# Optimization experiments

Hardware: AMD Instinct MI355X
Metric: run time of the kernel (lower is better)

Reference implementation:

```python
import jax, jax.numpy as jnp
import numpy as np

CUR, FULL, BS, DIM, H, D = 512, 1024, 4, 1024, 16, 64
PREV = FULL - CUR


def _rel_shift(x):
    # x: (cur, full, bs, h) -- TransformerXL relative shift (pad/reshape/slice)
    cur, full = x.shape[0], x.shape[1]
    zero_pad = jnp.zeros((cur, 1) + x.shape[2:], x.dtype)
    x_padded = jnp.concatenate([zero_pad, x], axis=1)           # (cur, full+1, bs, h)
    x_padded = x_padded.reshape((full + 1, cur) + x.shape[2:])  # view trick
    x = x_padded[1:].reshape(x.shape)
    tri = jnp.tril(jnp.ones((cur, full), x.dtype), full - cur)  # keep valid band
    return x * tri[:, :, None, None]


def setup_inputs() -> dict:
    key = jax.random.key(0)
    ks = jax.random.split(key, 12)
    s = jnp.float32(0.02)
    # causal mask: query i (at absolute pos i+PREV) may not attend to key j > i+PREV
    mask = (jnp.arange(FULL)[None, :] > (jnp.arange(CUR)[:, None] + PREV))[:, :, None]
    return {
        "inputs": jax.random.normal(ks[0], (CUR, BS, DIM), jnp.float32),
        "pos_embedding": jax.random.normal(ks[1], (FULL, 1, DIM), jnp.float32),
        "full_input": jax.random.normal(ks[2], (FULL, BS, DIM), jnp.float32),
        "u": jax.random.normal(ks[3], (H, D), jnp.float32) * s,
        "v": jax.random.normal(ks[4], (H, D), jnp.float32) * s,
        "W_kv": jax.random.normal(ks[5], (DIM, 2 * H * D), jnp.float32) * s,
        "b_kv": jnp.zeros((2 * H * D,), jnp.float32),
        "W_q": jax.random.normal(ks[6], (DIM, H * D), jnp.float32) * s,
        "b_q": jnp.zeros((H * D,), jnp.float32),
        "W_pos": jax.random.normal(ks[7], (DIM, H * D), jnp.float32) * s,
        "b_pos": jnp.zeros((H * D,), jnp.float32),
        "W_proj": jax.random.normal(ks[8], (H * D, DIM), jnp.float32) * s,
        "b_proj": jnp.zeros((DIM,), jnp.float32),
        "mask": mask,
    }


def reference(inputs, pos_embedding, full_input, u, v, W_kv, b_kv, W_q, b_q,
              W_pos, b_pos, W_proj, b_proj, mask):
    cur_seq, bs = inputs.shape[0], inputs.shape[1]
    full_seq = full_input.shape[0]
    scale = jnp.float32(1.0 / D ** 0.5)

    kv = full_input @ W_kv + b_kv                       # (full, bs, 2*H*D)
    key, value = jnp.split(kv, 2, axis=-1)
    query = inputs @ W_q + b_q                          # (cur, bs, H*D)
    r = (pos_embedding @ W_pos + b_pos).reshape(full_seq, H, D)

    key = key.reshape(full_seq, bs, H, D)
    value = value.reshape(full_seq, bs, H, D)
    query = query.reshape(cur_seq, bs, H, D)

    content_attn = jnp.einsum('ibhd,jbhd->ijbh', query + u, key)
    position_attn = jnp.einsum('ibhd,jhd->ijbh', query + v, r)
    position_attn = _rel_shift(position_attn)

    attn = (content_attn + position_attn) * scale       # (cur, full, bs, h)
    attn = jnp.where(mask[:, :, :, None], -jnp.inf, attn)
    attn = jax.nn.softmax(attn, axis=1)                 # softmax over full_seq

    attn_vec = jnp.einsum('ijbh,jbhd->ibhd', attn, value)
    attn_vec = attn_vec.reshape(cur_seq, bs, H * D)
    return attn_vec @ W_proj + b_proj                   # (cur, bs, DIM)
```

## Files before the change

kernel.cpp:

```cpp
#include <hip/hip_runtime.h>


typedef unsigned short u16;
typedef short short8 __attribute__((ext_vector_type(8)));
typedef float f32x4 __attribute__((ext_vector_type(4)));

#define BSZ 4
#define PREV 512

__device__ __forceinline__ float b2f(u16 u) {
  union { unsigned int i; float f; } x; x.i = ((unsigned int)u) << 16; return x.f;
}
__device__ __forceinline__ u16 f2b(float f) {
  union { float f; unsigned int i; } x; x.f = f;
  unsigned int u = x.i;
  return (u16)((u + 0x7fffu + ((u >> 16) & 1u)) >> 16);
}
__device__ __forceinline__ void storeC(u16* C, size_t idx, float v) { C[idx] = f2b(v); }
__device__ __forceinline__ void storeC(float* C, size_t idx, float v) { C[idx] = v; }

__device__ __forceinline__ void load_lds16(const u16* g, void* l) {
  __builtin_amdgcn_global_load_lds(
      (const __attribute__((address_space(1))) unsigned int*)g,
      (__attribute__((address_space(3))) unsigned int*)l, 16, 0, 0);
}

__global__ __launch_bounds__(256)
void prep(const float* __restrict__ s0, const float* __restrict__ s1,
          const float* __restrict__ s2, u16* __restrict__ d0,
          u16* __restrict__ d1, u16* __restrict__ d2,
          const float* __restrict__ W0, const float* __restrict__ W1,
          const float* __restrict__ W2, const float* __restrict__ W3,
          u16* __restrict__ T0, u16* __restrict__ T1,
          u16* __restrict__ T2, u16* __restrict__ T3) {
  __shared__ u16 ld[64 * 66];
  const int bxg = blockIdx.x;
  if (bxg < 3584) {
    const float* s; u16* d; size_t base;
    if (bxg < 2048)      { s = s0; d = d0; base = (size_t)bxg * 2048; }
    else if (bxg < 3072) { s = s1; d = d1; base = (size_t)(bxg - 2048) * 2048; }
    else                 { s = s2; d = d2; base = (size_t)(bxg - 3072) * 2048; }
    size_t i = base + (size_t)threadIdx.x * 8;
    const f32x4* p = reinterpret_cast<const f32x4*>(s + i);
    f32x4 a = p[0], b = p[1];
    short8 r;
#pragma unroll
    for (int e = 0; e < 4; e++) { r[e] = (short)f2b(a[e]); r[e + 4] = (short)f2b(b[e]); }
    *reinterpret_cast<short8*>(d + i) = r;
    return;
  }
  const int l = bxg - 3584;
  const int z = l >> 9;
  const int rem = l & 511;
  const int bx = rem & 31, by = rem >> 5;
  const float* W; u16* T; int N;
  if (z == 0)      { W = W0; T = T0; N = 2048; }
  else if (z == 1) { W = W1; T = T1; N = 1024; }
  else if (z == 2) { W = W2; T = T2; N = 1024; }
  else             { W = W3; T = T3; N = 1024; }
  const int K = 1024;
  const int n0 = bx * 64, k0 = by * 64;
  if (n0 >= N) return;

  const int tid = threadIdx.x;
#pragma unroll
  for (int rep = 0; rep < 16; rep++) {
    int idx = tid + 256 * rep;
    int kk = idx >> 6, nn = idx & 63;
    ld[kk * 66 + nn] = f2b(W[(size_t)(k0 + kk) * N + n0 + nn]);
  }
  __syncthreads();
#pragma unroll
  for (int rep = 0; rep < 16; rep++) {
    int idx = tid + 256 * rep;
    int nn = idx >> 6, kk = idx & 63;
    T[(size_t)(n0 + nn) * K + k0 + kk] = ld[kk * 66 + nn];
  }
}

template <typename OT, int MODE>
__device__ __forceinline__ void gemm_core(
    short* __restrict__ at, short* __restrict__ bt,
    const u16* __restrict__ A, const u16* __restrict__ BT,
    const float* __restrict__ bias, OT* __restrict__ C, u16* __restrict__ C2,
    int N, int K, int bx, int by)
{
  const int tid = threadIdx.x;
  const int lane = tid & 63, w = tid >> 6;
  const int wr = w >> 1, wc = w & 1;
  const int quad = lane >> 4, ml = lane & 15;
  const int row0 = by * 128, col0 = bx * 128;

  const int srow = lane & 15;
  const int skoff = (lane >> 4) * 8;

  f32x4 acc[4][4];
  const f32x4 fzero = {0.f, 0.f, 0.f, 0.f};
#pragma unroll
  for (int i = 0; i < 4; i++)
#pragma unroll
    for (int j = 0; j < 4; j++) acc[i][j] = fzero;

  for (int k0 = 0; k0 < K; k0 += 64) {
    __syncthreads();
#pragma unroll
    for (int i = 0; i < 4; i++) {
      int c = 4 * w + i;
      int mc = c >> 1, kc = c & 1;
      load_lds16(A + (size_t)(row0 + mc * 16 + srow) * K + k0 + kc * 32 + skoff,
                 (void*)(at + c * 512));
      load_lds16(BT + (size_t)(col0 + mc * 16 + srow) * K + k0 + kc * 32 + skoff,
                 (void*)(bt + c * 512));
    }
    __syncthreads();

    short8 af[4][2], bf[4][2];
#pragma unroll
    for (int mc = 0; mc < 4; mc++)
#pragma unroll
      for (int kc = 0; kc < 2; kc++)
        af[mc][kc] = *reinterpret_cast<const short8*>(at + ((((wr * 4 + mc) * 2 + kc) * 64) + lane) * 8);
#pragma unroll
    for (int nc = 0; nc < 4; nc++)
#pragma unroll
      for (int kc = 0; kc < 2; kc++)
        bf[nc][kc] = *reinterpret_cast<const short8*>(bt + ((((wc * 4 + nc) * 2 + kc) * 64) + lane) * 8);

#pragma unroll
    for (int mc = 0; mc < 4; mc++)
#pragma unroll
      for (int nc = 0; nc < 4; nc++)
#pragma unroll
        for (int kc = 0; kc < 2; kc++)
          acc[mc][nc] = __builtin_amdgcn_mfma_f32_16x16x32_bf16(af[mc][kc], bf[nc][kc], acc[mc][nc], 0, 0, 0);
  }

#pragma unroll
  for (int nc = 0; nc < 4; nc++) {
    int col = col0 + wc * 64 + nc * 16 + ml;
    float bv = bias[col];
#pragma unroll
    for (int mc = 0; mc < 4; mc++) {
#pragma unroll
      for (int reg = 0; reg < 4; reg++) {
        int row = row0 + wr * 64 + mc * 16 + quad * 4 + reg;
        float val = acc[mc][nc][reg] + bv;
        if constexpr (MODE == 0) {
          storeC(C, (size_t)row * N + col, val);
        } else if constexpr (MODE == 1) {
          int j = row >> 2, bb = row & 3;
          int tile = j >> 6, jl = j & 63;
          if (col < 1024) {
            int h = col >> 6, d = col & 63;
            int ncj = jl >> 4, nlj = jl & 15, kcd = d >> 5, qdd = (d >> 3) & 3, jjd = d & 7;
            C[((size_t)(bb * 16 + h) * 16 + tile) * 4096 +
              ((ncj * 2 + kcd) * 64 + qdd * 16 + nlj) * 8 + jjd] = f2b(val);
          } else {
            int c2 = col - 1024;
            int h = c2 >> 6, d = c2 & 63;
            int ncd = d >> 4, nld = d & 15, kcj = jl >> 5, qdj = (jl >> 3) & 3, jjj = jl & 7;
            C2[((size_t)(bb * 16 + h) * 16 + tile) * 4096 +
               ((kcj * 4 + ncd) * 64 + qdj * 16 + nld) * 8 + jjj] = f2b(val);
          }
        } else {
          int h = col >> 6, d = col & 63;
          C[((size_t)h * 1024 + row) * 64 + d] = f2b(val);
        }
      }
    }
  }
}

__global__ __launch_bounds__(256, 2)
void gemm3(const u16* __restrict__ fibf, const u16* __restrict__ WkvT,
           const float* __restrict__ b_kv, u16* __restrict__ Kt2, u16* __restrict__ Vt2,
           const u16* __restrict__ inbf, const u16* __restrict__ WqT,
           const float* __restrict__ b_q, u16* __restrict__ qq,
           const u16* __restrict__ pebf, const u16* __restrict__ WposT,
           const float* __restrict__ b_pos, u16* __restrict__ Rt)
{
  __shared__ __align__(16) short at[8192];
  __shared__ __align__(16) short bt[8192];
  const int id = blockIdx.x;
  if (id < 512) {
    gemm_core<u16, 1>(at, bt, fibf, WkvT, b_kv, Kt2, Vt2, 2048, 1024, id & 15, id >> 4);
  } else if (id < 640) {
    const int l = id - 512;
    gemm_core<u16, 0>(at, bt, inbf, WqT, b_q, qq, (u16*)nullptr, 1024, 1024, l & 7, l >> 3);
  } else {
    const int l = id - 640;
    gemm_core<u16, 2>(at, bt, pebf, WposT, b_pos, Rt, (u16*)nullptr, 1024, 1024, l & 7, l >> 3);
  }
}

__global__ __launch_bounds__(256, 2)
void gemm_proj(const u16* __restrict__ A, const u16* __restrict__ BT,
               const float* __restrict__ bias, float* __restrict__ C)
{
  __shared__ __align__(16) short at[8192];
  __shared__ __align__(16) short bt[8192];
  gemm_core<float, 0>(at, bt, A, BT, bias, C, (u16*)nullptr, 1024, 1024,
                      blockIdx.x, blockIdx.y);
}

__global__ __launch_bounds__(256, 4)
void flash_xl(const u16* __restrict__ q, const u16* __restrict__ Kt2,
              const u16* __restrict__ Vt2, const u16* __restrict__ Rt,
              const float* __restrict__ u, const float* __restrict__ v,
              float* __restrict__ po, float* __restrict__ pm,
              float* __restrict__ pl)
{
  __shared__ __align__(16) short kb[4096];
  __shared__ __align__(16) short vb[4096];
  __shared__ __align__(16) short pt[4][1024];

  const int tid = threadIdx.x, lane = tid & 63, w = tid >> 6;
  const int quad = lane >> 4, ml = lane & 15;
  const int x = blockIdx.x;
  int it, s, nseg;
  if (x < 12) { int g = x / 3; it = 7 - g; s = x - g * 3; nseg = 3; }
  else        { int y = x - 12; it = 3 - (y >> 1); s = y & 1; nseg = 2; }
  const int nt = it + 9;
  const int qn = (nseg == 3) ? (nt / 3) : (nt >> 1);
  const int rn = nt - qn * nseg;
  const int ts = s * qn + (s < rn ? s : rn);
  const int te = ts + qn + (s < rn ? 1 : 0);

  const int b = blockIdx.y, h = blockIdx.z;
  const int bh = b * 16 + h;
  const int i0 = it * 64, ig0 = i0 + w * 16;

  const u16* Kbase = Kt2 + ((size_t)(b * 16 + h) * 16) * 4096;
  const u16* Vbase = Vt2 + ((size_t)(b * 16 + h) * 16) * 4096;
  const u16* Rp = Rt + (size_t)h * 65536;

  short8 qu[2], qvf[2];
  {
    int ig = ig0 + ml;
#pragma unroll
    for (int kc = 0; kc < 2; kc++) {
      int dbase = kc * 32 + quad * 8;
      short8 qq = *reinterpret_cast<const short8*>(q + ((size_t)ig * BSZ + b) * 1024 + h * 64 + dbase);
      const f32x4* up = reinterpret_cast<const f32x4*>(u + h * 64 + dbase);
      const f32x4* vp = reinterpret_cast<const f32x4*>(v + h * 64 + dbase);
      f32x4 u0 = up[0], u1 = up[1], v0 = vp[0], v1 = vp[1];
#pragma unroll
      for (int e = 0; e < 8; e++) {
        float qf = b2f((u16)qq[e]);
        float uu = (e < 4) ? u0[e] : u1[e - 4];
        float vv = (e < 4) ? v0[e] : v1[e - 4];
        qu[kc][e]  = (short)f2b((qf + uu) * 0.125f);
        qvf[kc][e] = (short)f2b((qf + vv) * 0.125f);
      }
    }
  }

  const f32x4 fzero = {0.f, 0.f, 0.f, 0.f};
  f32x4 o_acc[4];
#pragma unroll
  for (int i = 0; i < 4; i++) o_acc[i] = fzero;
  float m_run[4], l_run[4];
#pragma unroll
  for (int i = 0; i < 4; i++) { m_run[i] = -1e30f; l_run[i] = 0.f; }

  short8 pk0, pk1, pv0, pv1;
  {
    const u16* kg = Kbase + (size_t)ts * 4096;
    const u16* vg = Vbase + (size_t)ts * 4096;
    pk0 = *reinterpret_cast<const short8*>(kg + tid * 8);
    pk1 = *reinterpret_cast<const short8*>(kg + 2048 + tid * 8);
    pv0 = *reinterpret_cast<const short8*>(vg + tid * 8);
    pv1 = *reinterpret_cast<const short8*>(vg + 2048 + tid * 8);
  }

  for (int t = ts; t < te; t++) {
    const int j0 = t * 64;
    __syncthreads();
    *reinterpret_cast<short8*>(kb + tid * 8) = pk0;
    *reinterpret_cast<short8*>(kb + 2048 + tid * 8) = pk1;
    *reinterpret_cast<short8*>(vb + tid * 8) = pv0;
    *reinterpret_cast<short8*>(vb + 2048 + tid * 8) = pv1;
    __syncthreads();

    if (t + 1 < te) {
      const u16* kg = Kbase + (size_t)(t + 1) * 4096;
      const u16* vg = Vbase + (size_t)(t + 1) * 4096;
      pk0 = *reinterpret_cast<const short8*>(kg + tid * 8);
      pk1 = *reinterpret_cast<const short8*>(kg + 2048 + tid * 8);
      pv0 = *reinterpret_cast<const short8*>(vg + tid * 8);
      pv1 = *reinterpret_cast<const short8*>(vg + 2048 + tid * 8);
    }

    f32x4 sc[4];
#pragma unroll
    for (int nc = 0; nc < 4; nc++) {
      sc[nc] = fzero;
#pragma unroll
      for (int kc = 0; kc < 2; kc++) {
        short8 kf = *reinterpret_cast<const short8*>(kb + ((nc * 2 + kc) * 64 + lane) * 8);
        sc[nc] = __builtin_amdgcn_mfma_f32_16x16x32_bf16(qu[kc], kf, sc[nc], 0, 0, 0);
      }
    }
    const int relstart = j0 - ig0 + 496;
    f32x4 p2[5];
#pragma unroll
    for (int c = 0; c < 5; c++) {
      p2[c] = fzero;
      int rel = relstart + c * 16 + ml;
      if (rel > 1023) rel = 1023;
      const u16* rp = Rp + (size_t)rel * 64 + quad * 8;
#pragma unroll
      for (int kc = 0; kc < 2; kc++) {
        short8 rf = *reinterpret_cast<const short8*>(rp + kc * 32);
        p2[c] = __builtin_amdgcn_mfma_f32_16x16x32_bf16(qvf[kc], rf, p2[c], 0, 0, 0);
      }
    }

    const bool anymask = (j0 + 63) > (ig0 + PREV);
    float pv_[4][4];
    float tmax[4] = {-1e30f, -1e30f, -1e30f, -1e30f};
#pragma unroll
    for (int reg = 0; reg < 4; reg++) {
      int rowl = quad * 4 + reg;
      int src = quad * 16 + ((ml - rowl - 1) & 15);
      bool hi = ml > rowl;
      float sh[5];
#pragma unroll
      for (int c = 0; c < 5; c++) sh[c] = __shfl(p2[c][reg], src, 64);
#pragma unroll
      for (int nc = 0; nc < 4; nc++) {
        float sv = sc[nc][reg] + (hi ? sh[nc + 1] : sh[nc]);
        if (anymask) {
          int jg = j0 + nc * 16 + ml;
          if (jg > ig0 + rowl + PREV) sv = -1e30f;
        }
        pv_[nc][reg] = sv;
        tmax[reg] = fmaxf(tmax[reg], sv);
      }
    }
#pragma unroll
    for (int reg = 0; reg < 4; reg++) {
      float tm = tmax[reg];
#pragma unroll
      for (int off = 1; off < 16; off <<= 1) tm = fmaxf(tm, __shfl_xor(tm, off, 64));
      float mnew = fmaxf(m_run[reg], tm);
      float alpha = __expf(m_run[reg] - mnew);
      float rs = 0.f;
#pragma unroll
      for (int nc = 0; nc < 4; nc++) {
        float p = __expf(pv_[nc][reg] - mnew);
        pv_[nc][reg] = p;
        rs += p;
      }
#pragma unroll
      for (int off = 1; off < 16; off <<= 1) rs += __shfl_xor(rs, off, 64);
      l_run[reg] = l_run[reg] * alpha + rs;
      m_run[reg] = mnew;
#pragma unroll
      for (int nc = 0; nc < 4; nc++) o_acc[nc][reg] *= alpha;
    }

#pragma unroll
    for (int nc = 0; nc < 4; nc++) {
      int jl = nc * 16 + ml;
      int kc = nc >> 1, qdj = (jl >> 3) & 3, jj = ml & 7;
#pragma unroll
      for (int reg = 0; reg < 4; reg++) {
        int rowl = quad * 4 + reg;
        pt[w][(kc * 64 + qdj * 16 + rowl) * 8 + jj] = (short)f2b(pv_[nc][reg]);
      }
    }
    short8 pf[2];
    pf[0] = *reinterpret_cast<const short8*>(pt[w] + (0 * 64 + lane) * 8);
    pf[1] = *reinterpret_cast<const short8*>(pt[w] + (1 * 64 + lane) * 8);

#pragma unroll
    for (int ncd = 0; ncd < 4; ncd++)
#pragma unroll
      for (int kc = 0; kc < 2; kc++) {
        short8 vf = *reinterpret_cast<const short8*>(vb + ((kc * 4 + ncd) * 64 + lane) * 8);
        o_acc[ncd] = __builtin_amdgcn_mfma_f32_16x16x32_bf16(pf[kc], vf, o_acc[ncd], 0, 0, 0);
      }
  }

#pragma unroll
  for (int reg = 0; reg < 4; reg++) {
    int ig = ig0 + quad * 4 + reg;
    size_t ridx = (s < 2) ? ((size_t)(s * 512 + ig) * 64 + bh)
                          : ((size_t)65536 + (size_t)(ig - 256) * 64 + bh);
    if (ml == 0) { pm[ridx] = m_run[reg]; pl[ridx] = l_run[reg]; }
#pragma unroll
    for (int ncd = 0; ncd < 4; ncd++)
      po[ridx * 64 + ncd * 16 + ml] = o_acc[ncd][reg];
  }
}

__global__ __launch_bounds__(256)
void combine(const float* __restrict__ po, const float* __restrict__ pm,
             const float* __restrict__ pl, u16* __restrict__ av) {
  int idx = blockIdx.x * 256 + threadIdx.x;
  int d = idx & 63;
  int r0 = idx >> 6;
  int ig = r0 >> 6;
  float m1 = pm[r0], m2 = pm[32768 + r0];
  float l1 = pl[r0], l2 = pl[32768 + r0];
  float o1 = po[(size_t)r0 * 64 + d];
  float o2 = po[((size_t)32768 + r0) * 64 + d];
  float m = fmaxf(m1, m2);
  const bool h3 = ig >= 256;
  int r2 = r0 + 49152;
  float m3 = -1e30f, l3 = 0.f, o3 = 0.f;
  if (h3) { m3 = pm[r2]; l3 = pl[r2]; o3 = po[(size_t)r2 * 64 + d]; m = fmaxf(m, m3); }
  float a1 = __expf(m1 - m), a2 = __expf(m2 - m);
  float l = l1 * a1 + l2 * a2;
  float o = o1 * a1 + o2 * a2;
  if (h3) { float a3 = __expf(m3 - m); l += l3 * a3; o += o3 * a3; }
  av[(size_t)r0 * 64 + d] = f2b(o / l);
}

extern "C" void kernel_launch(void* const* d_in, const int* in_sizes, int n_in,
                              void* d_out, int out_size, void* d_ws, size_t ws_size,
                              hipStream_t stream) {
  (void)in_sizes; (void)n_in; (void)out_size; (void)ws_size;

  const float* inputs  = (const float*)d_in[0];
  const float* pos_emb = (const float*)d_in[1];
  const float* full_in = (const float*)d_in[2];
  const float* u       = (const float*)d_in[3];
  const float* v       = (const float*)d_in[4];
  const float* W_kv    = (const float*)d_in[5];
  const float* b_kv    = (const float*)d_in[6];
  const float* W_q     = (const float*)d_in[7];
  const float* b_q     = (const float*)d_in[8];
  const float* W_pos   = (const float*)d_in[9];
  const float* b_pos   = (const float*)d_in[10];
  const float* W_proj  = (const float*)d_in[11];
  const float* b_proj  = (const float*)d_in[12];
  float* out = (float*)d_out;

  char* ws = (char*)d_ws;
  u16* Kt2   = (u16*)(ws);
  u16* Vt2   = (u16*)(ws + ( 8u << 20));
  u16* qq    = (u16*)(ws + (16u << 20));
  u16* Rt    = (u16*)(ws + (20u << 20));
  u16* av    = (u16*)(ws + (22u << 20));
  u16* WkvT  = (u16*)(ws + (26u << 20));
  u16* WqT   = (u16*)(ws + (30u << 20));
  u16* WposT = (u16*)(ws + (32u << 20));
  u16* WprojT= (u16*)(ws + (34u << 20));
  u16* fibf  = (u16*)(ws + (36u << 20));
  u16* inbf  = (u16*)(ws + (44u << 20));
  u16* pebf  = (u16*)(ws + (48u << 20));
  float* po  = (float*)(ws + (36u << 20));
  float* pm  = (float*)(ws + (56u << 20));
  float* pl  = (float*)(ws + (57u << 20));

  hipLaunchKernelGGL(prep, dim3(5632), dim3(256), 0, stream,
                     full_in, inputs, pos_emb, fibf, inbf, pebf,
                     W_kv, W_q, W_pos, W_proj, WkvT, WqT, WposT, WprojT);

  hipLaunchKernelGGL(gemm3, dim3(704), dim3(256), 0, stream,
                     fibf, WkvT, b_kv, Kt2, Vt2,
                     inbf, WqT, b_q, qq,
                     pebf, WposT, b_pos, Rt);

  hipLaunchKernelGGL(flash_xl, dim3(20, 4, 16), dim3(256), 0, stream,
                     qq, Kt2, Vt2, Rt, u, v, po, pm, pl);
  hipLaunchKernelGGL(combine, dim3(8192), dim3(256), 0, stream, po, pm, pl, av);

  hipLaunchKernelGGL(gemm_proj, dim3(8, 16), dim3(256), 0, stream,
                     av, WprojT, b_proj, out);
}
```

Baseline: 258.0 us.

## Store GEMM operands pre-tiled so LDS loads read contiguous 1KB chunks

The prep kernel and the combine kernel now write bf16 GEMM operands (activations, transposed weights, attention output) in a blocked 16-row by 32-k tile layout. Each global_load_lds then fetches a contiguous 1KB chunk instead of sixteen strided 64-byte row segments. The combine kernel is also vectorized to 8 elements per thread, cutting its grid by 8x. The cost is a scattered-write transpose in prep, and every consumer must agree on the new layout.

After: 231.5 us. -10.3%, faster.

```diff
diff --git a/kernel.cpp b/kernel.cpp
--- a/kernel.cpp
+++ b/kernel.cpp
@@ -23,6 +23,11 @@
   __builtin_amdgcn_global_load_lds(
       (const __attribute__((address_space(1))) unsigned int*)g,
       (__attribute__((address_space(3))) unsigned int*)l, 16, 0, 0);
+}
+
+__device__ __forceinline__ size_t pidx8(int row, int k, int K32) {
+  return (((size_t)((row >> 4) * K32 + (k >> 5))) << 9) +
+         (((k >> 3) & 3) << 7) + ((row & 15) << 3);
 }
 
 __global__ __launch_bounds__(256)
@@ -46,7 +51,8 @@
     short8 r;
 #pragma unroll
     for (int e = 0; e < 4; e++) { r[e] = (short)f2b(a[e]); r[e + 4] = (short)f2b(b[e]); }
-    *reinterpret_cast<short8*>(d + i) = r;
+    int row = (int)(i >> 10), k = (int)(i & 1023);
+    *reinterpret_cast<short8*>(d + pidx8(row, k, 32)) = r;
     return;
   }
   const int l = bxg - 3584;
@@ -58,7 +64,6 @@
   else if (z == 1) { W = W1; T = T1; N = 1024; }
   else if (z == 2) { W = W2; T = T2; N = 1024; }
   else             { W = W3; T = T3; N = 1024; }
-  const int K = 1024;
   const int n0 = bx * 64, k0 = by * 64;
   if (n0 >= N) return;
 
@@ -71,10 +76,13 @@
   }
   __syncthreads();
 #pragma unroll
-  for (int rep = 0; rep < 16; rep++) {
+  for (int rep = 0; rep < 2; rep++) {
     int idx = tid + 256 * rep;
-    int nn = idx >> 6, kk = idx & 63;
-    T[(size_t)(n0 + nn) * K + k0 + kk] = ld[kk * 66 + nn];
+    int nn = idx >> 3, k8 = (idx & 7) * 8;
+    short8 r;
+#pragma unroll
+    for (int e = 0; e < 8; e++) r[e] = (short)ld[(k8 + e) * 66 + nn];
+    *reinterpret_cast<short8*>(T + pidx8(n0 + nn, k0 + k8, 32)) = r;
   }
 }
 
@@ -90,9 +98,7 @@
   const int wr = w >> 1, wc = w & 1;
   const int quad = lane >> 4, ml = lane & 15;
   const int row0 = by * 128, col0 = bx * 128;
-
-  const int srow = lane & 15;
-  const int skoff = (lane >> 4) * 8;
+  const int K32 = K >> 5;
 
   f32x4 acc[4][4];
   const f32x4 fzero = {0.f, 0.f, 0.f, 0.f};
@@ -107,10 +113,10 @@
     for (int i = 0; i < 4; i++) {
       int c = 4 * w + i;
       int mc = c >> 1, kc = c & 1;
-      load_lds16(A + (size_t)(row0 + mc * 16 + srow) * K + k0 + kc * 32 + skoff,
-                 (void*)(at + c * 512));
-      load_lds16(BT + (size_t)(col0 + mc * 16 + srow) * K + k0 + kc * 32 + skoff,
-                 (void*)(bt + c * 512));
+      size_t ca = ((size_t)(((row0 >> 4) + mc) * K32 + (k0 >> 5) + kc)) << 9;
+      size_t cb = ((size_t)(((col0 >> 4) + mc) * K32 + (k0 >> 5) + kc)) << 9;
+      load_lds16(A + ca + lane * 8, (void*)(at + c * 512));
+      load_lds16(BT + cb + lane * 8, (void*)(bt + c * 512));
     }
     __syncthreads();
 
@@ -398,24 +404,36 @@
 __global__ __launch_bounds__(256)
 void combine(const float* __restrict__ po, const float* __restrict__ pm,
              const float* __restrict__ pl, u16* __restrict__ av) {
-  int idx = blockIdx.x * 256 + threadIdx.x;
-  int d = idx & 63;
-  int r0 = idx >> 6;
-  int ig = r0 >> 6;
+  int t = blockIdx.x * 256 + threadIdx.x;
+  int r0 = t >> 3, d8 = (t & 7) * 8;
+  int ig = r0 >> 6, b = (r0 >> 4) & 3, h = r0 & 15;
   float m1 = pm[r0], m2 = pm[32768 + r0];
   float l1 = pl[r0], l2 = pl[32768 + r0];
-  float o1 = po[(size_t)r0 * 64 + d];
-  float o2 = po[((size_t)32768 + r0) * 64 + d];
+  const f32x4* p1 = reinterpret_cast<const f32x4*>(po + (size_t)r0 * 64 + d8);
+  const f32x4* p2 = reinterpret_cast<const f32x4*>(po + ((size_t)32768 + r0) * 64 + d8);
+  f32x4 o1a = p1[0], o1b = p1[1], o2a = p2[0], o2b = p2[1];
   float m = fmaxf(m1, m2);
   const bool h3 = ig >= 256;
   int r2 = r0 + 49152;
-  float m3 = -1e30f, l3 = 0.f, o3 = 0.f;
-  if (h3) { m3 = pm[r2]; l3 = pl[r2]; o3 = po[(size_t)r2 * 64 + d]; m = fmaxf(m, m3); }
+  float m3 = -1e30f, l3 = 0.f;
+  f32x4 o3a = {0.f, 0.f, 0.f, 0.f}, o3b = {0.f, 0.f, 0.f, 0.f};
+  if (h3) {
+    m3 = pm[r2]; l3 = pl[r2];
+    const f32x4* p3 = reinterpret_cast<const f32x4*>(po + (size_t)r2 * 64 + d8);
+    o3a = p3[0]; o3b = p3[1];
+    m = fmaxf(m, m3);
+  }
   float a1 = __expf(m1 - m), a2 = __expf(m2 - m);
-  float l = l1 * a1 + l2 * a2;
-  float o = o1 * a1 + o2 * a2;
-  if (h3) { float a3 = __expf(m3 - m); l += l3 * a3; o += o3 * a3; }
-  av[(size_t)r0 * 64 + d] = f2b(o / l);
+  float a3 = h3 ? __expf(m3 - m) : 0.f;
+  float l = l1 * a1 + l2 * a2 + l3 * a3;
+  short8 r;
+#pragma unroll
+  for (int e = 0; e < 4; e++) {
+    r[e]     = (short)f2b((o1a[e] * a1 + o2a[e] * a2 + o3a[e] * a3) / l);
+    r[e + 4] = (short)f2b((o1b[e] * a1 + o2b[e] * a2 + o3b[e] * a3) / l);
+  }
+  int row = ig * 4 + b, k = h * 64 + d8;
+  *reinterpret_cast<short8*>(av + pidx8(row, k, 32)) = r;
 }
 
 extern "C" void kernel_launch(void* const* d_in, const int* in_sizes, int n_in,
@@ -466,7 +484,7 @@
 
   hipLaunchKernelGGL(flash_xl, dim3(20, 4, 16), dim3(256), 0, stream,
                      qq, Kt2, Vt2, Rt, u, v, po, pm, pl);
-  hipLaunchKernelGGL(combine, dim3(8192), dim3(256), 0, stream, po, pm, pl, av);
+  hipLaunchKernelGGL(combine, dim3(1024), dim3(256), 0, stream, po, pm, pl, av);
 
   hipLaunchKernelGGL(gemm_proj, dim3(8, 16), dim3(256), 0, stream,
                      av, WprojT, b_proj, out);
```
